# Kernel optimization log

Hardware: AMD Instinct MI355X
Metric: run time of the kernel (lower is better)

The kernel has to match this reference:

```python
import jax, jax.numpy as jnp
import numpy as np

ALPHA = 0.9
EPS = 0.01
LAMBDA_PENALTY = 1.0
THRESHOLD = 0.8
COS_EPS = 1e-8
N, F, E = 8192, 256, 262144


def setup_inputs() -> dict:
    key = jax.random.key(0)
    k1, k2, k3, k4, k5 = jax.random.split(key, 5)
    z = jax.random.normal(k1, (N, F), dtype=jnp.float32)
    x_hat = jax.random.normal(k2, (N, F), dtype=jnp.float32)
    edge_index = jax.random.randint(k3, (2, E), 0, N, dtype=jnp.int64)
    f_k2u = jax.random.randint(k4, (N,), 0, 6, dtype=jnp.int64)
    f_u2k = jax.random.randint(k5, (N,), 0, 32, dtype=jnp.int64)
    return {"z": z, "x_hat": x_hat, "edge_index": edge_index,
            "f_k2u": f_k2u, "f_u2k": f_u2k, "epoch": 10}


def _corrcoef_features(z):
    # torch.corrcoef(z.T): correlation between the F feature columns over N nodes
    zm = z - jnp.mean(z, axis=0, keepdims=True)        # [N, F]
    cov = zm.T @ zm                                    # [F, F] (scale cancels in corr)
    std = jnp.sqrt(jnp.diag(cov))                      # [F]
    cor = cov / (std[:, None] * std[None, :])
    cor = jnp.clip(jnp.nan_to_num(cor), -1.0, 1.0)
    # fill_diagonal_(0)
    return cor * (1.0 - jnp.eye(cor.shape[0], dtype=cor.dtype))


def reference(z, x_hat, edge_index, f_k2u, f_u2k, epoch):
    n, f = z.shape
    zm = z - jnp.mean(z, axis=0, keepdims=True)
    cor = _corrcoef_features(z)                        # [F, F]
    # per-node scalar weight: alpha**f_k2u + (1 - alpha**f_u2k)
    w = (ALPHA ** f_k2u.astype(z.dtype)
         + (1.0 - ALPHA ** f_u2k.astype(z.dtype)))     # [N]
    W = w[:, None] * zm                                # [N, F]
    z2 = z + EPS * (W @ cor)                           # [N, F]

    # homophily (crash=True): per-edge cosine sim, scatter-add by source, degree-normalize
    i, j = edge_index[0], edge_index[1]
    zi, zj = z2[i], z2[j]                              # [E, F] gathers
    num = jnp.sum(zi * zj, axis=1)
    ni = jnp.maximum(jnp.linalg.norm(zi, axis=1), COS_EPS)
    nj = jnp.maximum(jnp.linalg.norm(zj, axis=1), COS_EPS)
    sim = num / (ni * nj)                              # [E]
    scores = jax.ops.segment_sum(sim, i, num_segments=n)
    deg = jax.ops.segment_sum(jnp.ones_like(sim), i, num_segments=n)
    deg = jnp.where(deg == 0, 1.0, deg)
    homophily_loss = -jnp.mean(scores / deg)

    # extra_loss (crash=True): dense NxN similarity masked by dense adjacency
    sim_mat = z2 @ z2.T                                # [N, N]
    adj = jnp.zeros((n, n), dtype=z.dtype)
    adj = adj.at[i, j].set(1.0).at[j, i].set(1.0)
    non_conn = sim_mat * (1.0 - adj)
    penalty = jnp.mean(jnp.where(non_conn > THRESHOLD, non_conn, 0.0))

    return homophily_loss + LAMBDA_PENALTY * penalty
```

## Files before the change

### kernel.cpp

```cpp
#include <hip/hip_runtime.h>
#include <stdint.h>
#include <math.h>

#define EPS_C 0.01f
#define THRESH 0.8f

constexpr int Nn = 8192;
constexpr int Ff = 256;
constexpr int Ee = 262144;

__device__ __forceinline__ float b2f(unsigned short u) {
  union { uint32_t i; float f; } v; v.i = ((uint32_t)u) << 16; return v.f;
}
__device__ __forceinline__ unsigned short f2b(float f) {
  union { uint32_t i; float f; } v; v.f = f;
  uint32_t r = v.i + 0x7FFFu + ((v.i >> 16) & 1u);
  return (unsigned short)(r >> 16);
}

typedef __bf16 bf16x8 __attribute__((ext_vector_type(8)));
typedef float f32x4 __attribute__((ext_vector_type(4)));

__global__ void k_transpose(const float* __restrict__ z, unsigned short* __restrict__ zT,
                            float* __restrict__ colsum) {
  __shared__ float Ls[64][65];
  int n0 = blockIdx.x * 64;
  int c0 = blockIdx.y * 64;
  int t = threadIdx.x;
  int r = t >> 4;
  int cq = t & 15;
#pragma unroll
  for (int i = 0; i < 4; ++i) {
    int row = r + 16 * i;
    float4 v = *(const float4*)(z + (size_t)(n0 + row) * Ff + c0 + cq * 4);
    Ls[row][cq * 4 + 0] = v.x;
    Ls[row][cq * 4 + 1] = v.y;
    Ls[row][cq * 4 + 2] = v.z;
    Ls[row][cq * 4 + 3] = v.w;
  }
  __syncthreads();
  if (t < 64) {
    float s = 0.f;
#pragma unroll
    for (int rr = 0; rr < 64; ++rr) s += Ls[rr][t];
    atomicAdd(&colsum[c0 + t], s);
  }
  int cr = t >> 4;
  int nq = t & 15;
#pragma unroll
  for (int i = 0; i < 4; ++i) {
    int c = cr + 16 * i;
    ushort4 o;
    o.x = f2b(Ls[nq * 4 + 0][c]);
    o.y = f2b(Ls[nq * 4 + 1][c]);
    o.z = f2b(Ls[nq * 4 + 2][c]);
    o.w = f2b(Ls[nq * 4 + 3][c]);
    *(ushort4*)(zT + (size_t)(c0 + c) * Nn + n0 + nq * 4) = o;
  }
}

__global__ __launch_bounds__(256, 2) void k_covg(const unsigned short* __restrict__ zT,
                                                 float* __restrict__ covp) {
  int bx = blockIdx.x, by = blockIdx.y, p = blockIdx.z;
  __shared__ __align__(16) unsigned short As[128 * 64];
  __shared__ __align__(16) unsigned short Bs[128 * 64];
  int t = threadIdx.x;
  int lane = t & 63, wv = t >> 6;
  int wr = wv >> 1, wc = wv & 1;
  int quad = lane >> 4, l15 = lane & 15;
  int a0 = by * 128, b0 = bx * 128;

  f32x4 acc[4][4];
#pragma unroll
  for (int i = 0; i < 4; ++i)
#pragma unroll
    for (int j = 0; j < 4; ++j) acc[i][j] = (f32x4){0.f, 0.f, 0.f, 0.f};

  for (int kk = 0; kk < 8; ++kk) {
    int k0 = p * 512 + kk * 64;
#pragma unroll
    for (int it = 0; it < 4; ++it) {
      int s = it * 256 + t;
      int r = s >> 3;
      int g = (s & 7) ^ (r & 7);
      const unsigned short* ga = zT + (size_t)(a0 + r) * Nn + k0 + g * 8;
      const unsigned short* gb = zT + (size_t)(b0 + r) * Nn + k0 + g * 8;
      __builtin_amdgcn_global_load_lds((const __attribute__((address_space(1))) void*)ga,
                                       (__attribute__((address_space(3))) void*)(As + s * 8),
                                       16, 0, 0);
      __builtin_amdgcn_global_load_lds((const __attribute__((address_space(1))) void*)gb,
                                       (__attribute__((address_space(3))) void*)(Bs + s * 8),
                                       16, 0, 0);
    }
    __syncthreads();
#pragma unroll
    for (int kc = 0; kc < 2; ++kc) {
      bf16x8 afr[4], bfr[4];
#pragma unroll
      for (int mt = 0; mt < 4; ++mt) {
        int rA = wr * 64 + mt * 16 + l15;
        int g = kc * 4 + quad;
        int gl = g ^ (rA & 7);
        afr[mt] = *(const bf16x8*)(As + ((size_t)rA * 8 + gl) * 8);
      }
#pragma unroll
      for (int nt = 0; nt < 4; ++nt) {
        int rB = wc * 64 + nt * 16 + l15;
        int g = kc * 4 + quad;
        int gl = g ^ (rB & 7);
        bfr[nt] = *(const bf16x8*)(Bs + ((size_t)rB * 8 + gl) * 8);
      }
#pragma unroll
      for (int mt = 0; mt < 4; ++mt)
#pragma unroll
        for (int nt = 0; nt < 4; ++nt)
          acc[mt][nt] = __builtin_amdgcn_mfma_f32_16x16x32_bf16(afr[mt], bfr[nt],
                                                                acc[mt][nt], 0, 0, 0);
    }
    __syncthreads();
  }

  float* outp = covp + (size_t)p * 65536;
#pragma unroll
  for (int mt = 0; mt < 4; ++mt)
#pragma unroll
    for (int r = 0; r < 4; ++r) {
      int a = a0 + wr * 64 + mt * 16 + quad * 4 + r;
#pragma unroll
      for (int nt = 0; nt < 4; ++nt) {
        int b = b0 + wc * 64 + nt * 16 + l15;
        outp[(size_t)a * Ff + b] = acc[mt][nt][r];
      }
    }
}

__global__ void k_cor(const float* __restrict__ covp, const float* __restrict__ colsum,
                      float* __restrict__ cor) {
  __shared__ float sd[256];
  int a = blockIdx.x, b = threadIdx.x;
  float mb = colsum[b] * (1.f / 8192.f);
  float gb = 0.f;
#pragma unroll
  for (int p = 0; p < 16; ++p) gb += covp[(size_t)p * 65536 + b * 257];
  float sb = sqrtf(gb - 8192.f * mb * mb);
  sd[b] = sb;
  float g = 0.f;
#pragma unroll
  for (int p = 0; p < 16; ++p) g += covp[(size_t)p * 65536 + a * Ff + b];
  __syncthreads();
  float c = 0.f;
  if (a != b) {
    float ma = colsum[a] * (1.f / 8192.f);
    float cv = g - 8192.f * ma * mb;
    c = cv / (sd[a] * sb);
    if (c != c) c = 0.f;
    c = fminf(1.f, fmaxf(-1.f, c));
  }
  cor[a * Ff + b] = c;
}

__global__ __launch_bounds__(256) void k_z2(const float* __restrict__ z,
    const float* __restrict__ colsum, const int* __restrict__ k2u,
    const int* __restrict__ u2k, const float* __restrict__ cor,
    unsigned short* __restrict__ z2b, float* __restrict__ norms) {
  __shared__ float Wl[32 * 256];
  __shared__ float ws_[32];
  int t = threadIdx.x;
  int row0 = blockIdx.x * 32;
  if (t < 32) {
    int row = row0 + t;
    ws_[t] = powf(0.9f, (float)k2u[row]) + 1.f - powf(0.9f, (float)u2k[row]);
  }
  __syncthreads();
  float mt = colsum[t] * (1.f / 8192.f);
  for (int rr = 0; rr < 32; ++rr) {
    int row = row0 + rr;
    Wl[rr * 256 + t] = ws_[rr] * (z[(size_t)row * Ff + t] - mt);
  }
  __syncthreads();
  int tc = t & 63, tr = t >> 6;
  float acc[8][4];
#pragma unroll
  for (int i = 0; i < 8; ++i)
#pragma unroll
    for (int j = 0; j < 4; ++j) acc[i][j] = 0.f;
  const float* corc = cor + tc * 4;
  for (int k = 0; k < 256; ++k) {
    float4 c4 = *(const float4*)(corc + (size_t)k * 256);
#pragma unroll
    for (int rr = 0; rr < 8; ++rr) {
      float wv = Wl[(tr * 8 + rr) * 256 + k];
      acc[rr][0] = fmaf(wv, c4.x, acc[rr][0]);
      acc[rr][1] = fmaf(wv, c4.y, acc[rr][1]);
      acc[rr][2] = fmaf(wv, c4.z, acc[rr][2]);
      acc[rr][3] = fmaf(wv, c4.w, acc[rr][3]);
    }
  }
#pragma unroll
  for (int rr = 0; rr < 8; ++rr) {
    int row = row0 + tr * 8 + rr;
    float4 zv = *(const float4*)(z + (size_t)row * Ff + tc * 4);
    float x0 = zv.x + EPS_C * acc[rr][0];
    float x1 = zv.y + EPS_C * acc[rr][1];
    float x2 = zv.z + EPS_C * acc[rr][2];
    float x3 = zv.w + EPS_C * acc[rr][3];
    ushort4 o;
    o.x = f2b(x0); o.y = f2b(x1); o.z = f2b(x2); o.w = f2b(x3);
    *(ushort4*)(z2b + (size_t)row * Ff + tc * 4) = o;
    float s = x0 * x0 + x1 * x1 + x2 * x2 + x3 * x3;
#pragma unroll
    for (int m = 1; m < 64; m <<= 1) s += __shfl_xor(s, m);
    if (tc == 0) norms[row] = fmaxf(sqrtf(s), 1e-8f);
  }
}

__global__ void k_adj(const int* __restrict__ ei, const int* __restrict__ ej,
                      unsigned int* __restrict__ adj) {
  int e = blockIdx.x * 256 + threadIdx.x;
  unsigned int i = (unsigned int)ei[e], j = (unsigned int)ej[e];
  size_t b1 = (size_t)i * Nn + j;
  size_t b2 = (size_t)j * Nn + i;
  atomicOr(&adj[b1 >> 5], 1u << (b1 & 31));
  atomicOr(&adj[b2 >> 5], 1u << (b2 & 31));
}

__global__ __launch_bounds__(256) void k_edge(const int* __restrict__ ei,
                       const int* __restrict__ ej,
                       const unsigned short* __restrict__ z2b,
                       const float* __restrict__ norms,
                       float* __restrict__ scores, float* __restrict__ deg) {
  int t = threadIdx.x;
  int wv = t >> 6, lane = t & 63;
  int half = lane >> 5;
  int l32 = lane & 31;
  int gw = blockIdx.x * 4 + wv;
  int ebase = gw * 32;
#pragma unroll 2
  for (int it = 0; it < 16; ++it) {
    int e = ebase + it * 2 + half;
    int i = ei[e], j = ej[e];
    uint4 ua = *(const uint4*)(z2b + (size_t)i * Ff + l32 * 8);
    uint4 ub = *(const uint4*)(z2b + (size_t)j * Ff + l32 * 8);
    float d = 0.f;
    const uint32_t* pa = (const uint32_t*)&ua;
    const uint32_t* pb = (const uint32_t*)&ub;
#pragma unroll
    for (int q = 0; q < 4; ++q) {
      union { uint32_t u; float f; } alo, ahi, blo, bhi;
      alo.u = pa[q] << 16;  ahi.u = pa[q] & 0xffff0000u;
      blo.u = pb[q] << 16;  bhi.u = pb[q] & 0xffff0000u;
      d = fmaf(alo.f, blo.f, d);
      d = fmaf(ahi.f, bhi.f, d);
    }
#pragma unroll
    for (int m = 1; m < 32; m <<= 1) d += __shfl_xor(d, m);
    if (l32 == 0) {
      float sim = d / (norms[i] * norms[j]);
      atomicAdd(&scores[i], sim);
      atomicAdd(&deg[i], 1.f);
    }
  }
}

__global__ __launch_bounds__(256, 2) void k_penalty(const unsigned short* __restrict__ z2b,
    const unsigned int* __restrict__ adj, float* __restrict__ pp) {
  int tb = blockIdx.x;
  int br = (int)(64.5 - sqrt(64.5 * 64.5 - 2.0 * (double)tb));
  while ((br + 1) * 64 - ((br + 1) * br) / 2 <= tb) ++br;
  while (br * 64 - (br * (br - 1)) / 2 > tb) --br;
  int bc = br + (tb - (br * 64 - (br * (br - 1)) / 2));

  __shared__ __align__(16) unsigned short LB[32768];
  int t = threadIdx.x;
  int lane = t & 63;
  int wv = t >> 6;
  int wr = wv >> 1, wc = wv & 1;
  int quad = lane >> 4;
  int l15 = lane & 15;
  int arow0 = br * 128, brow0 = bc * 128;

  f32x4 acc[4][4];
#pragma unroll
  for (int i = 0; i < 4; ++i)
#pragma unroll
    for (int j = 0; j < 4; ++j) acc[i][j] = (f32x4){0.f, 0.f, 0.f, 0.f};

#define ISSUE_PHASE(p)                                                                   \
  {                                                                                      \
    unsigned short* buf = LB + ((p) & 1) * 16384;                                        \
    int k0 = (p) * 64;                                                                   \
    _Pragma("unroll")                                                                    \
    for (int it = 0; it < 4; ++it) {                                                     \
      int s = it * 256 + t;                                                              \
      int r = s >> 3;                                                                    \
      int g = (s & 7) ^ (r & 7);                                                         \
      const unsigned short* ga = z2b + (size_t)(arow0 + r) * Ff + k0 + g * 8;            \
      const unsigned short* gb = z2b + (size_t)(brow0 + r) * Ff + k0 + g * 8;            \
      __builtin_amdgcn_global_load_lds((const __attribute__((address_space(1))) void*)ga,\
                                       (__attribute__((address_space(3))) void*)(buf + s * 8),      \
                                       16, 0, 0);                                        \
      __builtin_amdgcn_global_load_lds((const __attribute__((address_space(1))) void*)gb,\
                                       (__attribute__((address_space(3))) void*)(buf + 8192 + s * 8),\
                                       16, 0, 0);                                        \
    }                                                                                    \
  }

  ISSUE_PHASE(0)
  ISSUE_PHASE(1)
#pragma unroll
  for (int p = 0; p < 4; ++p) {
    if (p < 3) __builtin_amdgcn_s_waitcnt(0xF78);
    else       __builtin_amdgcn_s_waitcnt(0xF70);
    __builtin_amdgcn_s_barrier();
    const unsigned short* As = LB + (p & 1) * 16384;
    const unsigned short* Bs = As + 8192;
#pragma unroll
    for (int kc = 0; kc < 2; ++kc) {
      bf16x8 afr[4], bfr[4];
#pragma unroll
      for (int mt = 0; mt < 4; ++mt) {
        int rA = wr * 64 + mt * 16 + l15;
        int g = kc * 4 + quad;
        int gl = g ^ (rA & 7);
        afr[mt] = *(const bf16x8*)(As + ((size_t)rA * 8 + gl) * 8);
      }
#pragma unroll
      for (int nt = 0; nt < 4; ++nt) {
        int rB = wc * 64 + nt * 16 + l15;
        int g = kc * 4 + quad;
        int gl = g ^ (rB & 7);
        bfr[nt] = *(const bf16x8*)(Bs + ((size_t)rB * 8 + gl) * 8);
      }
#pragma unroll
      for (int mt = 0; mt < 4; ++mt)
#pragma unroll
        for (int nt = 0; nt < 4; ++nt)
          acc[mt][nt] = __builtin_amdgcn_mfma_f32_16x16x32_bf16(afr[mt], bfr[nt],
                                                                acc[mt][nt], 0, 0, 0);
    }
    __builtin_amdgcn_s_barrier();
    if (p < 2) ISSUE_PHASE(p + 2)
  }
#undef ISSUE_PHASE

  float local = 0.f;
  int a_base = arow0 + wr * 64;
  int b_base = brow0 + wc * 64;
#pragma unroll
  for (int mt = 0; mt < 4; ++mt) {
#pragma unroll
    for (int r = 0; r < 4; ++r) {
      int a = a_base + mt * 16 + quad * 4 + r;
      uint64_t bits = *(const uint64_t*)(adj + (size_t)a * 256 + (b_base >> 5));
#pragma unroll
      for (int nt = 0; nt < 4; ++nt) {
        float v = acc[mt][nt][r];
        int boff = nt * 16 + l15;
        bool conn = (bits >> boff) & 1ull;
        float wgt;
        if (br != bc) wgt = 2.f;
        else {
          int b = b_base + boff;
          wgt = (a < b) ? 2.f : (a == b ? 1.f : 0.f);
        }
        if (!conn && v > THRESH) local += wgt * v;
      }
    }
  }
#pragma unroll
  for (int m = 1; m < 64; m <<= 1) local += __shfl_xor(local, m);
  float* red = (float*)LB;
  if (lane == 0) red[wv] = local;
  __syncthreads();
  if (t == 0) pp[tb] = red[0] + red[1] + red[2] + red[3];
}

__global__ void k_final(const float* __restrict__ scores, const float* __restrict__ deg,
                        const float* __restrict__ pp, float* __restrict__ out) {
  __shared__ float redh[4];
  __shared__ float redp[4];
  int t = threadIdx.x;
  float acch = 0.f;
#pragma unroll 4
  for (int it = 0; it < 32; ++it) {
    int n = it * 256 + t;
    float dg = deg[n];
    acch += scores[n] / (dg == 0.f ? 1.f : dg);
  }
  float accp = 0.f;
#pragma unroll
  for (int it = 0; it < 9; ++it) {
    int idx = it * 256 + t;
    if (idx < 2080) accp += pp[idx];
  }
#pragma unroll
  for (int m = 1; m < 64; m <<= 1) {
    acch += __shfl_xor(acch, m);
    accp += __shfl_xor(accp, m);
  }
  if ((t & 63) == 0) { redh[t >> 6] = acch; redp[t >> 6] = accp; }
  __syncthreads();
  if (t == 0) {
    double h = -(double)(redh[0] + redh[1] + redh[2] + redh[3]) / 8192.0;
    double p = (double)(redp[0] + redp[1] + redp[2] + redp[3]) / (8192.0 * 8192.0);
    out[0] = (float)(h + p);
  }
}

extern "C" void kernel_launch(void* const* d_in, const int* in_sizes, int n_in,
                              void* d_out, int out_size, void* d_ws, size_t ws_size,
                              hipStream_t stream) {
  const float* z = (const float*)d_in[0];
  const int* ei = (const int*)d_in[2];
  const int* ej = ei + Ee;
  const int* k2u = (const int*)d_in[3];
  const int* u2k = (const int*)d_in[4];

  char* ws = (char*)d_ws;
  unsigned int* adj = (unsigned int*)(ws);
  float* colsum     = (float*)(ws + 8388608);
  float* scores     = (float*)(ws + 8389632);
  float* deg        = (float*)(ws + 8422400);
  const size_t ZERO_BYTES = 8455168;
  float* covp       = (float*)(ws + 8455296);
  unsigned short* zT  = (unsigned short*)(ws + 12649600);
  unsigned short* z2b = (unsigned short*)(ws + 16843904);
  float* cor        = (float*)(ws + 21038208);
  float* norms      = (float*)(ws + 21300352);
  float* pp         = (float*)(ws + 21333120);

  hipMemsetAsync(d_ws, 0, ZERO_BYTES, stream);
  k_adj<<<1024, 256, 0, stream>>>(ei, ej, adj);
  k_transpose<<<dim3(128, 4), 256, 0, stream>>>(z, zT, colsum);
  k_covg<<<dim3(2, 2, 16), 256, 0, stream>>>(zT, covp);
  k_cor<<<256, 256, 0, stream>>>(covp, colsum, cor);
  k_z2<<<256, 256, 0, stream>>>(z, colsum, k2u, u2k, cor, z2b, norms);
  k_edge<<<2048, 256, 0, stream>>>(ei, ej, z2b, norms, scores, deg);
  k_penalty<<<2080, 256, 0, stream>>>(z2b, adj, pp);
  k_final<<<1, 256, 0, stream>>>(scores, deg, pp, (float*)d_out);
}
```

Before: 217.8 us.

## Switch penalty Gram matrix to FP8 MFMA and halve z2 rows per block

```diff
diff --git a/kernel.cpp b/kernel.cpp
--- a/kernel.cpp
+++ b/kernel.cpp
@@ -162,34 +162,36 @@
 __global__ __launch_bounds__(256) void k_z2(const float* __restrict__ z,
     const float* __restrict__ colsum, const int* __restrict__ k2u,
     const int* __restrict__ u2k, const float* __restrict__ cor,
-    unsigned short* __restrict__ z2b, float* __restrict__ norms) {
-  __shared__ float Wl[32 * 256];
-  __shared__ float ws_[32];
-  int t = threadIdx.x;
-  int row0 = blockIdx.x * 32;
-  if (t < 32) {
+    unsigned short* __restrict__ z2b, unsigned char* __restrict__ z2f8,
+    float* __restrict__ norms) {
+  __shared__ float Wl[16 * 256];
+  __shared__ float ws_[16];
+  int t = threadIdx.x;
+  int row0 = blockIdx.x * 16;
+  if (t < 16) {
     int row = row0 + t;
     ws_[t] = powf(0.9f, (float)k2u[row]) + 1.f - powf(0.9f, (float)u2k[row]);
   }
   __syncthreads();
   float mt = colsum[t] * (1.f / 8192.f);
-  for (int rr = 0; rr < 32; ++rr) {
+#pragma unroll
+  for (int rr = 0; rr < 16; ++rr) {
     int row = row0 + rr;
     Wl[rr * 256 + t] = ws_[rr] * (z[(size_t)row * Ff + t] - mt);
   }
   __syncthreads();
   int tc = t & 63, tr = t >> 6;
-  float acc[8][4];
-#pragma unroll
-  for (int i = 0; i < 8; ++i)
+  float acc[4][4];
+#pragma unroll
+  for (int i = 0; i < 4; ++i)
 #pragma unroll
     for (int j = 0; j < 4; ++j) acc[i][j] = 0.f;
   const float* corc = cor + tc * 4;
   for (int k = 0; k < 256; ++k) {
     float4 c4 = *(const float4*)(corc + (size_t)k * 256);
 #pragma unroll
-    for (int rr = 0; rr < 8; ++rr) {
-      float wv = Wl[(tr * 8 + rr) * 256 + k];
+    for (int rr = 0; rr < 4; ++rr) {
+      float wv = Wl[(tr * 4 + rr) * 256 + k];
       acc[rr][0] = fmaf(wv, c4.x, acc[rr][0]);
       acc[rr][1] = fmaf(wv, c4.y, acc[rr][1]);
       acc[rr][2] = fmaf(wv, c4.z, acc[rr][2]);
@@ -197,8 +199,8 @@
     }
   }
 #pragma unroll
-  for (int rr = 0; rr < 8; ++rr) {
-    int row = row0 + tr * 8 + rr;
+  for (int rr = 0; rr < 4; ++rr) {
+    int row = row0 + tr * 4 + rr;
     float4 zv = *(const float4*)(z + (size_t)row * Ff + tc * 4);
     float x0 = zv.x + EPS_C * acc[rr][0];
     float x1 = zv.y + EPS_C * acc[rr][1];
@@ -207,6 +209,9 @@
     ushort4 o;
     o.x = f2b(x0); o.y = f2b(x1); o.z = f2b(x2); o.w = f2b(x3);
     *(ushort4*)(z2b + (size_t)row * Ff + tc * 4) = o;
+    int pk = __builtin_amdgcn_cvt_pk_fp8_f32(x0, x1, 0, 0);
+    pk = __builtin_amdgcn_cvt_pk_fp8_f32(x2, x3, pk, 1);
+    *(unsigned int*)(z2f8 + (size_t)row * Ff + tc * 4) = (unsigned int)pk;
     float s = x0 * x0 + x1 * x1 + x2 * x2 + x3 * x3;
 #pragma unroll
     for (int m = 1; m < 64; m <<= 1) s += __shfl_xor(s, m);
@@ -262,7 +267,7 @@
   }
 }
 
-__global__ __launch_bounds__(256, 2) void k_penalty(const unsigned short* __restrict__ z2b,
+__global__ __launch_bounds__(256, 4) void k_penalty(const unsigned char* __restrict__ z2f8,
     const unsigned int* __restrict__ adj, float* __restrict__ pp) {
   int tb = blockIdx.x;
   int br = (int)(64.5 - sqrt(64.5 * 64.5 - 2.0 * (double)tb));
@@ -270,7 +275,7 @@
   while (br * 64 - (br * (br - 1)) / 2 > tb) --br;
   int bc = br + (tb - (br * 64 - (br * (br - 1)) / 2));
 
-  __shared__ __align__(16) unsigned short LB[32768];
+  __shared__ __align__(16) unsigned char LB[32768];
   int t = threadIdx.x;
   int lane = t & 63;
   int wv = t >> 6;
@@ -287,20 +292,20 @@
 
 #define ISSUE_PHASE(p)                                                                   \
   {                                                                                      \
-    unsigned short* buf = LB + ((p) & 1) * 16384;                                        \
+    unsigned char* buf = LB + ((p) & 1) * 16384;                                         \
     int k0 = (p) * 64;                                                                   \
     _Pragma("unroll")                                                                    \
-    for (int it = 0; it < 4; ++it) {                                                     \
+    for (int it = 0; it < 2; ++it) {                                                     \
       int s = it * 256 + t;                                                              \
-      int r = s >> 3;                                                                    \
-      int g = (s & 7) ^ (r & 7);                                                         \
-      const unsigned short* ga = z2b + (size_t)(arow0 + r) * Ff + k0 + g * 8;            \
-      const unsigned short* gb = z2b + (size_t)(brow0 + r) * Ff + k0 + g * 8;            \
+      int r = s >> 2;                                                                    \
+      int gs = (s & 3) ^ (r & 3) ^ ((r >> 2) & 3);                                       \
+      const unsigned char* ga = z2f8 + (size_t)(arow0 + r) * Ff + k0 + gs * 16;          \
+      const unsigned char* gb = z2f8 + (size_t)(brow0 + r) * Ff + k0 + gs * 16;          \
       __builtin_amdgcn_global_load_lds((const __attribute__((address_space(1))) void*)ga,\
-                                       (__attribute__((address_space(3))) void*)(buf + s * 8),      \
+                                       (__attribute__((address_space(3))) void*)(buf + s * 16),      \
                                        16, 0, 0);                                        \
       __builtin_amdgcn_global_load_lds((const __attribute__((address_space(1))) void*)gb,\
-                                       (__attribute__((address_space(3))) void*)(buf + 8192 + s * 8),\
+                                       (__attribute__((address_space(3))) void*)(buf + 8192 + s * 16),\
                                        16, 0, 0);                                        \
     }                                                                                    \
   }
@@ -309,34 +314,34 @@
   ISSUE_PHASE(1)
 #pragma unroll
   for (int p = 0; p < 4; ++p) {
-    if (p < 3) __builtin_amdgcn_s_waitcnt(0xF78);
+    if (p < 3) __builtin_amdgcn_s_waitcnt(0xF74);
     else       __builtin_amdgcn_s_waitcnt(0xF70);
     __builtin_amdgcn_s_barrier();
-    const unsigned short* As = LB + (p & 1) * 16384;
-    const unsigned short* Bs = As + 8192;
+    const unsigned char* As = LB + (p & 1) * 16384;
+    const unsigned char* Bs = As + 8192;
 #pragma unroll
     for (int kc = 0; kc < 2; ++kc) {
-      bf16x8 afr[4], bfr[4];
+      long a8[4], b8[4];
+      int gidx = kc * 2 + (quad >> 1);
+      int bo = (quad & 1) * 8;
 #pragma unroll
       for (int mt = 0; mt < 4; ++mt) {
         int rA = wr * 64 + mt * 16 + l15;
-        int g = kc * 4 + quad;
-        int gl = g ^ (rA & 7);
-        afr[mt] = *(const bf16x8*)(As + ((size_t)rA * 8 + gl) * 8);
+        int gl = gidx ^ (rA & 3) ^ ((rA >> 2) & 3);
+        a8[mt] = *(const long*)(As + rA * 64 + gl * 16 + bo);
       }
 #pragma unroll
       for (int nt = 0; nt < 4; ++nt) {
         int rB = wc * 64 + nt * 16 + l15;
-        int g = kc * 4 + quad;
-        int gl = g ^ (rB & 7);
-        bfr[nt] = *(const bf16x8*)(Bs + ((size_t)rB * 8 + gl) * 8);
+        int gl = gidx ^ (rB & 3) ^ ((rB >> 2) & 3);
+        b8[nt] = *(const long*)(Bs + rB * 64 + gl * 16 + bo);
       }
 #pragma unroll
       for (int mt = 0; mt < 4; ++mt)
 #pragma unroll
         for (int nt = 0; nt < 4; ++nt)
-          acc[mt][nt] = __builtin_amdgcn_mfma_f32_16x16x32_bf16(afr[mt], bfr[nt],
-                                                                acc[mt][nt], 0, 0, 0);
+          acc[mt][nt] = __builtin_amdgcn_mfma_f32_16x16x32_fp8_fp8(a8[mt], b8[nt],
+                                                                   acc[mt][nt], 0, 0, 0);
     }
     __builtin_amdgcn_s_barrier();
     if (p < 2) ISSUE_PHASE(p + 2)
@@ -428,14 +433,15 @@
   float* cor        = (float*)(ws + 21038208);
   float* norms      = (float*)(ws + 21300352);
   float* pp         = (float*)(ws + 21333120);
+  unsigned char* z2f8 = (unsigned char*)(ws + 21341568);
 
   hipMemsetAsync(d_ws, 0, ZERO_BYTES, stream);
   k_adj<<<1024, 256, 0, stream>>>(ei, ej, adj);
   k_transpose<<<dim3(128, 4), 256, 0, stream>>>(z, zT, colsum);
   k_covg<<<dim3(2, 2, 16), 256, 0, stream>>>(zT, covp);
   k_cor<<<256, 256, 0, stream>>>(covp, colsum, cor);
-  k_z2<<<256, 256, 0, stream>>>(z, colsum, k2u, u2k, cor, z2b, norms);
+  k_z2<<<512, 256, 0, stream>>>(z, colsum, k2u, u2k, cor, z2b, z2f8, norms);
   k_edge<<<2048, 256, 0, stream>>>(ei, ej, z2b, norms, scores, deg);
-  k_penalty<<<2080, 256, 0, stream>>>(z2b, adj, pp);
+  k_penalty<<<2080, 256, 0, stream>>>(z2f8, adj, pp);
   k_final<<<1, 256, 0, stream>>>(scores, deg, pp, (float*)d_out);
 }
```

Result: faster. 209.1 us (-4.0%).
